# Kernel tuning notes

Measured on AMD Instinct MI355X. Metric: run time of the kernel, lower is better.

The kernel has to match this reference:

```python
import jax, jax.numpy as jnp
import numpy as np

N_NODES = 100000


def gcn_conv(x, edge_index, W, b, n):
    """PyG-style GCNConv: h = D^-1/2 (A + I) D^-1/2 (x W) + b."""
    h = x @ W  # [n, out]
    loops = jnp.arange(n, dtype=edge_index.dtype)
    src = jnp.concatenate([edge_index[0], loops])
    dst = jnp.concatenate([edge_index[1], loops])
    deg = jax.ops.segment_sum(jnp.ones_like(dst, dtype=h.dtype), dst, num_segments=n)
    dinv = jnp.where(deg > 0, jax.lax.rsqrt(deg), 0.0)
    norm = dinv[src] * dinv[dst]  # [E+n]
    msg = h[src] * norm[:, None]
    out = jax.ops.segment_sum(msg, dst, num_segments=n)
    return out + b


def setup_inputs() -> dict:
    key = jax.random.key(0)
    ks = jax.random.split(key, 12)
    n, f, hid, c, e = N_NODES, 128, 16, 32, 3200000
    x = jax.random.normal(ks[0], (n, f), dtype=jnp.float32)
    edge_index_pos = jax.random.randint(ks[1], (2, e), 0, n, dtype=jnp.int32)
    edge_index_neg = jax.random.randint(ks[2], (2, e), 0, n, dtype=jnp.int32)
    def glorot(k, fi, fo):
        lim = np.sqrt(6.0 / (fi + fo)).astype(np.float32)
        return jax.random.uniform(k, (fi, fo), minval=-lim, maxval=lim, dtype=jnp.float32)
    return {
        "x": x,
        "edge_index_pos": edge_index_pos,
        "edge_index_neg": edge_index_neg,
        "W1p": glorot(ks[3], f, hid), "b1p": jnp.zeros((hid,), jnp.float32),
        "W1n": glorot(ks[4], f, hid), "b1n": jnp.zeros((hid,), jnp.float32),
        "W2p": glorot(ks[5], hid, c), "b2p": jnp.zeros((c,), jnp.float32),
        "W2n": glorot(ks[6], hid, c), "b2n": jnp.zeros((c,), jnp.float32),
    }


def reference(x, edge_index_pos, edge_index_neg, W1p, b1p, W1n, b1n, W2p, b2p, W2n, b2n):
    n = x.shape[0]
    # layer 1: relu(pos) - relu(neg)
    h = (jax.nn.relu(gcn_conv(x, edge_index_pos, W1p, b1p, n))
         - jax.nn.relu(gcn_conv(x, edge_index_neg, W1n, b1n, n)))
    # dropout is identity in eval mode (training=False)
    h = (jax.nn.relu(gcn_conv(h, edge_index_pos, W2p, b2p, n))
         - jax.nn.relu(gcn_conv(h, edge_index_neg, W2n, b2n, n)))
    return jax.nn.log_softmax(h, axis=1)
```

## Files before the change

### kernel.cpp

```cpp
#include <hip/hip_runtime.h>
#include <hip/hip_fp16.h>


#define BSHIFT 8
#define BSZ 256
#define MAX_NBK 512
#define FILL_CAP 13056
#define SORT_CAP 12032

__device__ __forceinline__ int chunk_of_block(int bid, int NCH) {
  return (NCH % 8 == 0) ? (bid % 8) * (NCH / 8) + bid / 8 : bid;
}


__global__ __launch_bounds__(256) void bucket_count2(
    const int* __restrict__ eP, const int* __restrict__ eN,
    int E, int CH, int NCH, int NBK, int* __restrict__ ccP, int* __restrict__ ccN) {
  __shared__ int cnt[MAX_NBK];
  const int* dsts = (blockIdx.y ? eN : eP) + E;
  int* cc = blockIdx.y ? ccN : ccP;
  const int c = chunk_of_block(blockIdx.x, NCH);
  for (int i = threadIdx.x; i < NBK; i += 256) cnt[i] = 0;
  __syncthreads();
  int base = c * CH, end = min(E, base + CH);
  for (int idx = base + threadIdx.x; idx < end; idx += 256)
    atomicAdd(&cnt[dsts[idx] >> BSHIFT], 1);
  __syncthreads();
  for (int i = threadIdx.x; i < NBK; i += 256)
    cc[(size_t)c * NBK + i] = cnt[i];
}

__global__ __launch_bounds__(512) void col_scan2(
    int* __restrict__ ccP, int* __restrict__ ccN, int NCH, int NBK,
    int* __restrict__ totP, int* __restrict__ totN) {
  __shared__ int s[512];
  int* cc = blockIdx.y ? ccN : ccP;
  int* tot = blockIdx.y ? totN : totP;
  int b = blockIdx.x, t = threadIdx.x;
  int v = (t < NCH) ? cc[(size_t)t * NBK + b] : 0;
  s[t] = v;
  for (int off = 1; off < 512; off <<= 1) {
    __syncthreads();
    int a = (t >= off) ? s[t - off] : 0;
    __syncthreads();
    s[t] += a;
  }
  __syncthreads();
  if (t < NCH) cc[(size_t)t * NBK + b] = s[t] - v;
  if (t == 511) tot[b] = s[511];
}

__global__ __launch_bounds__(512) void base_scan(
    const int* __restrict__ totP, const int* __restrict__ totN, int NBK,
    int* __restrict__ baseP, int* __restrict__ baseN,
    int* __restrict__ rowP, int* __restrict__ rowN, int n, int E) {
  __shared__ int sp[512], sn[512];
  __shared__ int carryP, carryN;
  int t = threadIdx.x;
  if (t == 0) { carryP = 0; carryN = 0; }
  __syncthreads();
  for (int tile = 0; tile < NBK; tile += 512) {
    int idx = tile + t;
    int vp = (idx < NBK) ? totP[idx] : 0;
    int vn = (idx < NBK) ? totN[idx] : 0;
    sp[t] = vp; sn[t] = vn;
    for (int off = 1; off < 512; off <<= 1) {
      __syncthreads();
      int ap = (t >= off) ? sp[t - off] : 0;
      int an = (t >= off) ? sn[t - off] : 0;
      __syncthreads();
      sp[t] += ap; sn[t] += an;
    }
    __syncthreads();
    if (idx < NBK) {
      baseP[idx] = carryP + sp[t] - vp;
      baseN[idx] = carryN + sn[t] - vn;
    }
    __syncthreads();
    if (t == 0) { carryP += sp[511]; carryN += sn[511]; }
    __syncthreads();
  }
  if (t == 0) {
    baseP[NBK] = E; baseN[NBK] = E;
    rowP[n] = E; rowN[n] = E;
  }
}

__global__ __launch_bounds__(512) void bucket_fill3(
    const int* __restrict__ eP, const int* __restrict__ eN,
    int E, int CH, int NCH, int NBK,
    const int* __restrict__ ccP, const int* __restrict__ ccN,
    const int* __restrict__ totP, const int* __restrict__ totN,
    const int* __restrict__ basP, const int* __restrict__ basN,
    unsigned* __restrict__ prP, unsigned* __restrict__ prN) {
  __shared__ unsigned obuf[FILL_CAP];
  __shared__ int chofs[MAX_NBK], hist[MAX_NBK], lofs[MAX_NBK], cur[MAX_NBK];
  __shared__ int s[512];
  const int* edges = blockIdx.y ? eN : eP;
  const int* cc = blockIdx.y ? ccN : ccP;
  const int* tot = blockIdx.y ? totN : totP;
  const int* bas = blockIdx.y ? basN : basP;
  unsigned* pairs = blockIdx.y ? prN : prP;
  const int c = chunk_of_block(blockIdx.x, NCH);
  const int t = threadIdx.x;

  int h = 0;
  if (t < NBK) {
    int o0 = cc[(size_t)c * NBK + t];
    int o1 = (c + 1 < NCH) ? cc[(size_t)(c + 1) * NBK + t] : tot[t];
    chofs[t] = o0;
    h = o1 - o0;
    hist[t] = h;
  }
  s[t] = h;
  for (int off = 1; off < 512; off <<= 1) {
    __syncthreads();
    int a = (t >= off) ? s[t - off] : 0;
    __syncthreads();
    s[t] += a;
  }
  __syncthreads();
  if (t < NBK) { lofs[t] = s[t] - hist[t]; cur[t] = s[t] - hist[t]; }
  __syncthreads();

  int base = c * CH, end = min(E, base + CH);
  for (int idx = base + t; idx < end; idx += 512) {
    int sv = edges[idx], d = edges[E + idx];
    int b = d >> BSHIFT;
    int pos = atomicAdd(&cur[b], 1);
    obuf[pos] = (unsigned)sv | ((unsigned)(d & (BSZ - 1)) << 24);
  }
  __syncthreads();

  if (t < NBK) {
    int cnt = hist[t], lo = lofs[t];
    unsigned* dst = pairs + (size_t)bas[t] + chofs[t];
    for (int j = 0; j < cnt; ++j) dst[j] = obuf[lo + j];
  }
}

__global__ __launch_bounds__(256) void tile_sort3(
    const unsigned* __restrict__ prP, const unsigned* __restrict__ prN,
    const int* __restrict__ basP, const int* __restrict__ basN, int n,
    float* __restrict__ dinvP, float* __restrict__ dinvN,
    int* __restrict__ rowP, int* __restrict__ rowN,
    unsigned* __restrict__ srcsP, unsigned* __restrict__ srcsN) {
  __shared__ unsigned obuf[SORT_CAP];
  __shared__ int hist[BSZ];
  __shared__ int scn[BSZ];
  __shared__ int cur[BSZ];
  const unsigned* pairs = blockIdx.y ? prN : prP;
  const int* base = blockIdx.y ? basN : basP;
  float* dinv = blockIdx.y ? dinvN : dinvP;
  int* rowoff = blockIdx.y ? rowN : rowP;
  unsigned* srcs = blockIdx.y ? srcsN : srcsP;
  const int b = blockIdx.x, t = threadIdx.x;
  const int s0 = base[b], s1 = base[b + 1], cnt = s1 - s0;
  hist[t] = 0;
  __syncthreads();
  for (int i = s0 + t; i < s1; i += 256)
    atomicAdd(&hist[pairs[i] >> 24], 1);
  __syncthreads();
  scn[t] = hist[t];
  __syncthreads();
  for (int off = 1; off < BSZ; off <<= 1) {
    int v = (t >= off) ? scn[t - off] : 0;
    __syncthreads();
    scn[t] += v;
    __syncthreads();
  }
  {
    int excl = scn[t] - hist[t];
    cur[t] = excl;
    int node = b * BSZ + t;
    if (node < n) {
      rowoff[node] = s0 + excl;
      dinv[node] = rsqrtf(1.0f + (float)hist[t]);
    }
  }
  __syncthreads();
  if (cnt <= SORT_CAP) {
    for (int i = s0 + t; i < s1; i += 256) {
      unsigned p = pairs[i];
      int pos = atomicAdd(&cur[p >> 24], 1);
      obuf[pos] = p & 0xFFFFFFu;
    }
    __syncthreads();
    for (int i = t; i < cnt; i += 256) srcs[s0 + i] = obuf[i];
  } else {
    for (int i = s0 + t; i < s1; i += 256) {
      unsigned p = pairs[i];
      int pos = atomicAdd(&cur[p >> 24], 1);
      srcs[s0 + pos] = p & 0xFFFFFFu;
    }
  }
}

__global__ __launch_bounds__(256) void xw1_kernel(
    const float* __restrict__ x, const float* __restrict__ Wp, const float* __restrict__ Wn,
    const float* __restrict__ dinvP, const float* __restrict__ dinvN,
    __half* __restrict__ hp, __half* __restrict__ hn, int n)
{
  __shared__ float xs[16 * 132];
  __shared__ float wp[128 * 16], wn[128 * 16];
  const int tid = threadIdx.x;
  const int rowBase = blockIdx.x * 16;

  for (int idx = tid; idx < 512; idx += 256) {
    ((float4*)wp)[idx] = ((const float4*)Wp)[idx];
    ((float4*)wn)[idx] = ((const float4*)Wn)[idx];
  }
  const int nrows = min(16, n - rowBase);
  for (int idx = tid; idx < nrows * 32; idx += 256) {
    int r = idx >> 5, c4 = idx & 31;
    float4 v = ((const float4*)(x + (size_t)(rowBase + r) * 128))[c4];
    *(float4*)(xs + r * 132 + c4 * 4) = v;
  }
  __syncthreads();

  const int r = tid >> 4, c = tid & 15;
  const int i = rowBase + r;
  if (i < n) {
    float ap = 0.f, an = 0.f;
    #pragma unroll
    for (int k = 0; k < 128; ++k) {
      float xv = xs[r * 132 + k];
      ap += xv * wp[k * 16 + c];
      an += xv * wn[k * 16 + c];
    }
    hp[(size_t)i * 16 + c] = __float2half(ap * dinvP[i]);
    hn[(size_t)i * 16 + c] = __float2half(an * dinvN[i]);
  }
}

__device__ __forceinline__ void fma_mix2(float& aLo, float& aHi, unsigned h2, float one) {
  asm("v_fma_mix_f32 %0, %2, %3, %0 op_sel:[0,0,0] op_sel_hi:[1,0,0]\n\t"
      "v_fma_mix_f32 %1, %2, %3, %1 op_sel:[1,0,0] op_sel_hi:[1,0,0]"
      : "+v"(aLo), "+v"(aHi)
      : "v"(h2), "v"(one));
}

__device__ __forceinline__ void seg_sum4(
    const unsigned* __restrict__ srcs, int e, int e1,
    const __half* __restrict__ tab, int lane4, float one,
    float& f0, float& f1, float& f2, float& f3)
{
  float g0 = 0.f, g1 = 0.f, g2 = 0.f, g3 = 0.f;
  for (; e + 8 <= e1; e += 8) {
    unsigned a[8];
    #pragma unroll
    for (int j = 0; j < 8; ++j) a[j] = srcs[e + j];
    uint2 v[8];
    #pragma unroll
    for (int j = 0; j < 8; ++j)
      v[j] = *(const uint2*)(tab + (size_t)a[j] * 16 + lane4 * 4);
    #pragma unroll
    for (int j = 0; j < 8; j += 2) {
      fma_mix2(f0, f1, v[j].x, one);
      fma_mix2(f2, f3, v[j].y, one);
      fma_mix2(g0, g1, v[j + 1].x, one);
      fma_mix2(g2, g3, v[j + 1].y, one);
    }
  }
  for (; e + 2 <= e1; e += 2) {
    unsigned a0 = srcs[e], a1 = srcs[e + 1];
    uint2 v0 = *(const uint2*)(tab + (size_t)a0 * 16 + lane4 * 4);
    uint2 v1 = *(const uint2*)(tab + (size_t)a1 * 16 + lane4 * 4);
    fma_mix2(f0, f1, v0.x, one);
    fma_mix2(f2, f3, v0.y, one);
    fma_mix2(g0, g1, v1.x, one);
    fma_mix2(g2, g3, v1.y, one);
  }
  if (e < e1) {
    uint2 v = *(const uint2*)(tab + (size_t)srcs[e] * 16 + lane4 * 4);
    fma_mix2(f0, f1, v.x, one);
    fma_mix2(f2, f3, v.y, one);
  }
  f0 += g0; f1 += g1; f2 += g2; f3 += g3;
}

__global__ __launch_bounds__(256) void agg_split(
    const unsigned* __restrict__ srcP, const int* __restrict__ rowP,
    const unsigned* __restrict__ srcN, const int* __restrict__ rowN,
    const __half* __restrict__ inP, const __half* __restrict__ inN,
    const float* __restrict__ dinvP, const float* __restrict__ dinvN,
    float* __restrict__ tmpP, float* __restrict__ tmpN, int n)
{
  const int gb = blockIdx.x;
  const int xcd = gb & 7;
  const int sign = xcd >> 2;
  const int nblk = (gb >> 3) * 4 + (xcd & 3);
  const int lane4 = threadIdx.x & 3, grp = threadIdx.x >> 2;
  const int i = nblk * 64 + grp;
  if (i >= n) return;

  const unsigned* srcs = sign ? srcN : srcP;
  const int* row = sign ? rowN : rowP;
  const __half* tab = sign ? inN : inP;
  const float* dinv = sign ? dinvN : dinvP;
  float* tmp = sign ? tmpN : tmpP;

  const float one = 1.0f;
  float f0 = 0.f, f1 = 0.f, f2 = 0.f, f3 = 0.f;
  uint2 self = *(const uint2*)(tab + (size_t)i * 16 + lane4 * 4);
  fma_mix2(f0, f1, self.x, one);
  fma_mix2(f2, f3, self.y, one);
  seg_sum4(srcs, row[i], row[i + 1], tab, lane4, one, f0, f1, f2, f3);
  const float d = dinv[i];
  float4 o;
  o.x = f0 * d; o.y = f1 * d; o.z = f2 * d; o.w = f3 * d;
  *(float4*)(tmp + (size_t)i * 16 + lane4 * 4) = o;
}

__global__ __launch_bounds__(256) void combine1(
    const float* __restrict__ tmpP, const float* __restrict__ tmpN,
    const float* __restrict__ bp, const float* __restrict__ bn,
    const float* __restrict__ dinvP, const float* __restrict__ dinvN,
    __half* __restrict__ Gp, __half* __restrict__ Gn, long long total)
{
  long long j = (long long)blockIdx.x * 256 + threadIdx.x;
  if (j >= total) return;
  int i = (int)(j >> 4), lane = (int)(j & 15);
  float ap = bp[lane] + tmpP[j];
  float an = bn[lane] + tmpN[j];
  float h = fmaxf(ap, 0.f) - fmaxf(an, 0.f);
  Gp[j] = __float2half(h * dinvP[i]);
  Gn[j] = __float2half(h * dinvN[i]);
}

__global__ __launch_bounds__(256) void final2(
    const float* __restrict__ Up, const float* __restrict__ Un,
    const float* __restrict__ W2p, const float* __restrict__ W2n,
    const float* __restrict__ b2p, const float* __restrict__ b2n,
    float* __restrict__ out, int n)
{
  __shared__ float wp[16 * 32], wn[16 * 32];
  for (int i = threadIdx.x; i < 512; i += 256) { wp[i] = W2p[i]; wn[i] = W2n[i]; }
  __syncthreads();

  const int tid = threadIdx.x;
  const int lane = tid & 15, grp = tid >> 4;
  const int i = blockIdx.x * 16 + grp;
  if (i >= n) return;

  float tp = Up[(size_t)i * 16 + lane];
  float tn = Un[(size_t)i * 16 + lane];

  float ap0 = b2p[lane], ap1 = b2p[lane + 16];
  float an0 = b2n[lane], an1 = b2n[lane + 16];
  #pragma unroll
  for (int k = 0; k < 16; ++k) {
    float tpk = __shfl(tp, k, 16);
    float tnk = __shfl(tn, k, 16);
    ap0 += tpk * wp[k * 32 + lane];
    ap1 += tpk * wp[k * 32 + lane + 16];
    an0 += tnk * wn[k * 32 + lane];
    an1 += tnk * wn[k * 32 + lane + 16];
  }
  float v0 = fmaxf(ap0, 0.f) - fmaxf(an0, 0.f);
  float v1 = fmaxf(ap1, 0.f) - fmaxf(an1, 0.f);
  float m = fmaxf(v0, v1);
  #pragma unroll
  for (int off = 8; off > 0; off >>= 1) m = fmaxf(m, __shfl_xor(m, off, 16));
  float s = __expf(v0 - m) + __expf(v1 - m);
  #pragma unroll
  for (int off = 8; off > 0; off >>= 1) s += __shfl_xor(s, off, 16);
  float ls = __logf(s);
  out[(size_t)i * 32 + lane] = v0 - m - ls;
  out[(size_t)i * 32 + lane + 16] = v1 - m - ls;
}

extern "C" void kernel_launch(void* const* d_in, const int* in_sizes, int n_in,
                              void* d_out, int out_size, void* d_ws, size_t ws_size,
                              hipStream_t stream) {
  const float* x   = (const float*)d_in[0];
  const int*   eP  = (const int*)d_in[1];
  const int*   eN  = (const int*)d_in[2];
  const float* W1p = (const float*)d_in[3];
  const float* b1p = (const float*)d_in[4];
  const float* W1n = (const float*)d_in[5];
  const float* b1n = (const float*)d_in[6];
  const float* W2p = (const float*)d_in[7];
  const float* b2p = (const float*)d_in[8];
  const float* W2n = (const float*)d_in[9];
  const float* b2n = (const float*)d_in[10];
  float* out = (float*)d_out;

  const int HID = in_sizes[4];
  const int F   = in_sizes[3] / HID;
  const int n   = in_sizes[0] / F;
  const int E   = in_sizes[1] / 2;
  (void)out_size; (void)n_in; (void)ws_size;

  const int NBK = (n + BSZ - 1) >> BSHIFT;
  const int CH  = (((E + 255) / 256) + 255) & ~255;
  const int NCH = (E + CH - 1) / CH;

  char* p = (char*)d_ws;
  auto alloc = [&](size_t bytes) { char* r = p; p += (bytes + 255) & ~(size_t)255; return r; };

  int*      ccP   = (int*)alloc((size_t)NCH * NBK * 4);
  int*      ccN   = (int*)alloc((size_t)NCH * NBK * 4);
  int*      totP  = (int*)alloc((size_t)NBK * 4);
  int*      totN  = (int*)alloc((size_t)NBK * 4);
  int*      basP  = (int*)alloc((size_t)(NBK + 1) * 4);
  int*      basN  = (int*)alloc((size_t)(NBK + 1) * 4);
  unsigned* prP   = (unsigned*)alloc((size_t)E * 4);
  unsigned* prN   = (unsigned*)alloc((size_t)E * 4);
  unsigned* srcP  = (unsigned*)alloc((size_t)E * 4);
  unsigned* srcN  = (unsigned*)alloc((size_t)E * 4);
  int*      rowP  = (int*)alloc((size_t)(n + 1) * 4);
  int*      rowN  = (int*)alloc((size_t)(n + 1) * 4);
  float*    dinvP = (float*)alloc((size_t)n * 4);
  float*    dinvN = (float*)alloc((size_t)n * 4);
  __half*   hsP   = (__half*)alloc((size_t)n * 16 * 2);
  __half*   hsN   = (__half*)alloc((size_t)n * 16 * 2);
  __half*   Gp    = (__half*)alloc((size_t)n * 16 * 2);
  __half*   Gn    = (__half*)alloc((size_t)n * 16 * 2);
  float*    tmpP  = (float*)alloc((size_t)n * 16 * 4);
  float*    tmpN  = (float*)alloc((size_t)n * 16 * 4);

  hipLaunchKernelGGL(bucket_count2, dim3(NCH, 2), dim3(256), 0, stream,
                     eP, eN, E, CH, NCH, NBK, ccP, ccN);
  hipLaunchKernelGGL(col_scan2, dim3(NBK, 2), dim3(512), 0, stream,
                     ccP, ccN, NCH, NBK, totP, totN);
  hipLaunchKernelGGL(base_scan, dim3(1), dim3(512), 0, stream,
                     totP, totN, NBK, basP, basN, rowP, rowN, n, E);
  hipLaunchKernelGGL(bucket_fill3, dim3(NCH, 2), dim3(512), 0, stream,
                     eP, eN, E, CH, NCH, NBK, ccP, ccN, totP, totN,
                     basP, basN, prP, prN);
  hipLaunchKernelGGL(tile_sort3, dim3(NBK, 2), dim3(256), 0, stream,
                     prP, prN, basP, basN, n, dinvP, dinvN, rowP, rowN, srcP, srcN);

  const int NB16 = (n + 15) / 16;
  const int NB64 = (n + 63) / 64;
  const int NBS  = ((NB64 + 3) / 4) * 4;
  const int GRID = NBS * 2;

  hipLaunchKernelGGL(xw1_kernel, dim3(NB16), dim3(256), 0, stream,
                     x, W1p, W1n, dinvP, dinvN, hsP, hsN, n);
  hipLaunchKernelGGL(agg_split, dim3(GRID), dim3(256), 0, stream,
                     srcP, rowP, srcN, rowN, hsP, hsN, dinvP, dinvN, tmpP, tmpN, n);
  hipLaunchKernelGGL(combine1, dim3((int)(((long long)n * 16 + 255) / 256)), dim3(256), 0, stream,
                     tmpP, tmpN, b1p, b1n, dinvP, dinvN, Gp, Gn, (long long)n * 16);

  hipLaunchKernelGGL(agg_split, dim3(GRID), dim3(256), 0, stream,
                     srcP, rowP, srcN, rowN, Gp, Gn, dinvP, dinvN, tmpP, tmpN, n);
  hipLaunchKernelGGL(final2, dim3(NB16), dim3(256), 0, stream,
                     tmpP, tmpN, W2p, W2n, b2p, b2n, out, n);
}
```

Measured before the change: 241.1 us.

## Fold base scan into fill/sort kernels, vectorize edge loads, coalesce bucket writeback

Removes the single-block base_scan launch. bucket_fill3 now recomputes the bucket prefix locally, and tile_sort3 derives its start offset by reducing the preceding bucket totals. Edge loads in count and fill use nontemporal 4-wide loads. The per-bucket writeback in fill is spread across a wavefront instead of one thread per bucket, giving coalesced stores. combine1 is vectorized to float4 with packed half2 stores, and nontemporal hints are added to the aggregation loads and stores. The trade-off is redundant prefix work in every block; the tile_sort reduction grows with the bucket index, up to about 391 buckets.

```diff
diff --git a/kernel.cpp b/kernel.cpp
--- a/kernel.cpp
+++ b/kernel.cpp
@@ -7,6 +7,9 @@
 #define MAX_NBK 512
 #define FILL_CAP 13056
 #define SORT_CAP 12032
+
+typedef int   i32x4 __attribute__((ext_vector_type(4)));
+typedef float f32x4 __attribute__((ext_vector_type(4)));
 
 __device__ __forceinline__ int chunk_of_block(int bid, int NCH) {
   return (NCH % 8 == 0) ? (bid % 8) * (NCH / 8) + bid / 8 : bid;
@@ -23,8 +26,17 @@
   for (int i = threadIdx.x; i < NBK; i += 256) cnt[i] = 0;
   __syncthreads();
   int base = c * CH, end = min(E, base + CH);
-  for (int idx = base + threadIdx.x; idx < end; idx += 256)
-    atomicAdd(&cnt[dsts[idx] >> BSHIFT], 1);
+  for (int idx = base + threadIdx.x * 4; idx < end; idx += 1024) {
+    if (idx + 4 <= end) {
+      i32x4 d = __builtin_nontemporal_load((const i32x4*)(dsts + idx));
+      atomicAdd(&cnt[d.x >> BSHIFT], 1);
+      atomicAdd(&cnt[d.y >> BSHIFT], 1);
+      atomicAdd(&cnt[d.z >> BSHIFT], 1);
+      atomicAdd(&cnt[d.w >> BSHIFT], 1);
+    } else {
+      for (int k = idx; k < end; ++k) atomicAdd(&cnt[dsts[k] >> BSHIFT], 1);
+    }
+  }
   __syncthreads();
   for (int i = threadIdx.x; i < NBK; i += 256)
     cc[(size_t)c * NBK + i] = cnt[i];
@@ -50,56 +62,19 @@
   if (t == 511) tot[b] = s[511];
 }
 
-__global__ __launch_bounds__(512) void base_scan(
-    const int* __restrict__ totP, const int* __restrict__ totN, int NBK,
-    int* __restrict__ baseP, int* __restrict__ baseN,
-    int* __restrict__ rowP, int* __restrict__ rowN, int n, int E) {
-  __shared__ int sp[512], sn[512];
-  __shared__ int carryP, carryN;
-  int t = threadIdx.x;
-  if (t == 0) { carryP = 0; carryN = 0; }
-  __syncthreads();
-  for (int tile = 0; tile < NBK; tile += 512) {
-    int idx = tile + t;
-    int vp = (idx < NBK) ? totP[idx] : 0;
-    int vn = (idx < NBK) ? totN[idx] : 0;
-    sp[t] = vp; sn[t] = vn;
-    for (int off = 1; off < 512; off <<= 1) {
-      __syncthreads();
-      int ap = (t >= off) ? sp[t - off] : 0;
-      int an = (t >= off) ? sn[t - off] : 0;
-      __syncthreads();
-      sp[t] += ap; sn[t] += an;
-    }
-    __syncthreads();
-    if (idx < NBK) {
-      baseP[idx] = carryP + sp[t] - vp;
-      baseN[idx] = carryN + sn[t] - vn;
-    }
-    __syncthreads();
-    if (t == 0) { carryP += sp[511]; carryN += sn[511]; }
-    __syncthreads();
-  }
-  if (t == 0) {
-    baseP[NBK] = E; baseN[NBK] = E;
-    rowP[n] = E; rowN[n] = E;
-  }
-}
-
 __global__ __launch_bounds__(512) void bucket_fill3(
     const int* __restrict__ eP, const int* __restrict__ eN,
     int E, int CH, int NCH, int NBK,
     const int* __restrict__ ccP, const int* __restrict__ ccN,
     const int* __restrict__ totP, const int* __restrict__ totN,
-    const int* __restrict__ basP, const int* __restrict__ basN,
     unsigned* __restrict__ prP, unsigned* __restrict__ prN) {
   __shared__ unsigned obuf[FILL_CAP];
   __shared__ int chofs[MAX_NBK], hist[MAX_NBK], lofs[MAX_NBK], cur[MAX_NBK];
+  __shared__ int bas_l[MAX_NBK];
   __shared__ int s[512];
   const int* edges = blockIdx.y ? eN : eP;
   const int* cc = blockIdx.y ? ccN : ccP;
   const int* tot = blockIdx.y ? totN : totP;
-  const int* bas = blockIdx.y ? basN : basP;
   unsigned* pairs = blockIdx.y ? prN : prP;
   const int c = chunk_of_block(blockIdx.x, NCH);
   const int t = threadIdx.x;
@@ -123,25 +98,52 @@
   if (t < NBK) { lofs[t] = s[t] - hist[t]; cur[t] = s[t] - hist[t]; }
   __syncthreads();
 
+  int tv = (t < NBK) ? tot[t] : 0;
+  s[t] = tv;
+  for (int off = 1; off < 512; off <<= 1) {
+    __syncthreads();
+    int a = (t >= off) ? s[t - off] : 0;
+    __syncthreads();
+    s[t] += a;
+  }
+  __syncthreads();
+  if (t < NBK) bas_l[t] = s[t] - tv;
+  __syncthreads();
+
   int base = c * CH, end = min(E, base + CH);
-  for (int idx = base + t; idx < end; idx += 512) {
-    int sv = edges[idx], d = edges[E + idx];
-    int b = d >> BSHIFT;
-    int pos = atomicAdd(&cur[b], 1);
-    obuf[pos] = (unsigned)sv | ((unsigned)(d & (BSZ - 1)) << 24);
-  }
-  __syncthreads();
-
-  if (t < NBK) {
-    int cnt = hist[t], lo = lofs[t];
-    unsigned* dst = pairs + (size_t)bas[t] + chofs[t];
-    for (int j = 0; j < cnt; ++j) dst[j] = obuf[lo + j];
+  for (int idx = base + t * 4; idx < end; idx += 2048) {
+    if (idx + 4 <= end) {
+      i32x4 sv = __builtin_nontemporal_load((const i32x4*)(edges + idx));
+      i32x4 dv = __builtin_nontemporal_load((const i32x4*)(edges + E + idx));
+      int p0 = atomicAdd(&cur[dv.x >> BSHIFT], 1);
+      obuf[p0] = (unsigned)sv.x | ((unsigned)(dv.x & (BSZ - 1)) << 24);
+      int p1 = atomicAdd(&cur[dv.y >> BSHIFT], 1);
+      obuf[p1] = (unsigned)sv.y | ((unsigned)(dv.y & (BSZ - 1)) << 24);
+      int p2 = atomicAdd(&cur[dv.z >> BSHIFT], 1);
+      obuf[p2] = (unsigned)sv.z | ((unsigned)(dv.z & (BSZ - 1)) << 24);
+      int p3 = atomicAdd(&cur[dv.w >> BSHIFT], 1);
+      obuf[p3] = (unsigned)sv.w | ((unsigned)(dv.w & (BSZ - 1)) << 24);
+    } else {
+      for (int k = idx; k < end; ++k) {
+        int sv = edges[k], d = edges[E + k];
+        int pos = atomicAdd(&cur[d >> BSHIFT], 1);
+        obuf[pos] = (unsigned)sv | ((unsigned)(d & (BSZ - 1)) << 24);
+      }
+    }
+  }
+  __syncthreads();
+
+  const int wv = t >> 6, ln = t & 63;
+  for (int b = wv; b < NBK; b += 8) {
+    int cnt2 = hist[b], lo = lofs[b];
+    unsigned* dst = pairs + (size_t)bas_l[b] + chofs[b];
+    for (int j = ln; j < cnt2; j += 64) dst[j] = obuf[lo + j];
   }
 }
 
 __global__ __launch_bounds__(256) void tile_sort3(
     const unsigned* __restrict__ prP, const unsigned* __restrict__ prN,
-    const int* __restrict__ basP, const int* __restrict__ basN, int n,
+    const int* __restrict__ totP, const int* __restrict__ totN, int n, int E,
     float* __restrict__ dinvP, float* __restrict__ dinvN,
     int* __restrict__ rowP, int* __restrict__ rowN,
     unsigned* __restrict__ srcsP, unsigned* __restrict__ srcsN) {
@@ -149,17 +151,31 @@
   __shared__ int hist[BSZ];
   __shared__ int scn[BSZ];
   __shared__ int cur[BSZ];
+  __shared__ int red[256];
   const unsigned* pairs = blockIdx.y ? prN : prP;
-  const int* base = blockIdx.y ? basN : basP;
+  const int* tot = blockIdx.y ? totN : totP;
   float* dinv = blockIdx.y ? dinvN : dinvP;
   int* rowoff = blockIdx.y ? rowN : rowP;
   unsigned* srcs = blockIdx.y ? srcsN : srcsP;
   const int b = blockIdx.x, t = threadIdx.x;
-  const int s0 = base[b], s1 = base[b + 1], cnt = s1 - s0;
+
+  int part = 0;
+  for (int j = t; j < b; j += 256) part += tot[j];
+  red[t] = part;
+  __syncthreads();
+  for (int off = 128; off > 0; off >>= 1) {
+    if (t < off) red[t] += red[t + off];
+    __syncthreads();
+  }
+  const int s0 = red[0];
+  const int cnt = tot[b];
+  const int s1 = s0 + cnt;
+  if (b == (int)gridDim.x - 1 && t == 0) rowoff[n] = E;
+
   hist[t] = 0;
   __syncthreads();
   for (int i = s0 + t; i < s1; i += 256)
-    atomicAdd(&hist[pairs[i] >> 24], 1);
+    atomicAdd(&hist[__builtin_nontemporal_load(pairs + i) >> 24], 1);
   __syncthreads();
   scn[t] = hist[t];
   __syncthreads();
@@ -181,7 +197,7 @@
   __syncthreads();
   if (cnt <= SORT_CAP) {
     for (int i = s0 + t; i < s1; i += 256) {
-      unsigned p = pairs[i];
+      unsigned p = __builtin_nontemporal_load(pairs + i);
       int pos = atomicAdd(&cur[p >> 24], 1);
       obuf[pos] = p & 0xFFFFFFu;
     }
@@ -189,7 +205,7 @@
     for (int i = t; i < cnt; i += 256) srcs[s0 + i] = obuf[i];
   } else {
     for (int i = s0 + t; i < s1; i += 256) {
-      unsigned p = pairs[i];
+      unsigned p = __builtin_nontemporal_load(pairs + i);
       int pos = atomicAdd(&cur[p >> 24], 1);
       srcs[s0 + pos] = p & 0xFFFFFFu;
     }
@@ -249,7 +265,7 @@
   for (; e + 8 <= e1; e += 8) {
     unsigned a[8];
     #pragma unroll
-    for (int j = 0; j < 8; ++j) a[j] = srcs[e + j];
+    for (int j = 0; j < 8; ++j) a[j] = __builtin_nontemporal_load(srcs + e + j);
     uint2 v[8];
     #pragma unroll
     for (int j = 0; j < 8; ++j)
@@ -263,7 +279,8 @@
     }
   }
   for (; e + 2 <= e1; e += 2) {
-    unsigned a0 = srcs[e], a1 = srcs[e + 1];
+    unsigned a0 = __builtin_nontemporal_load(srcs + e);
+    unsigned a1 = __builtin_nontemporal_load(srcs + e + 1);
     uint2 v0 = *(const uint2*)(tab + (size_t)a0 * 16 + lane4 * 4);
     uint2 v1 = *(const uint2*)(tab + (size_t)a1 * 16 + lane4 * 4);
     fma_mix2(f0, f1, v0.x, one);
@@ -272,7 +289,8 @@
     fma_mix2(g2, g3, v1.y, one);
   }
   if (e < e1) {
-    uint2 v = *(const uint2*)(tab + (size_t)srcs[e] * 16 + lane4 * 4);
+    unsigned a0 = __builtin_nontemporal_load(srcs + e);
+    uint2 v = *(const uint2*)(tab + (size_t)a0 * 16 + lane4 * 4);
     fma_mix2(f0, f1, v.x, one);
     fma_mix2(f2, f3, v.y, one);
   }
@@ -294,11 +312,11 @@
   const int i = nblk * 64 + grp;
   if (i >= n) return;
 
-  const unsigned* srcs = sign ? srcN : srcP;
-  const int* row = sign ? rowN : rowP;
-  const __half* tab = sign ? inN : inP;
-  const float* dinv = sign ? dinvN : dinvP;
-  float* tmp = sign ? tmpN : tmpP;
+  const unsigned* __restrict__ srcs = sign ? srcN : srcP;
+  const int* __restrict__ row = sign ? rowN : rowP;
+  const __half* __restrict__ tab = sign ? inN : inP;
+  const float* __restrict__ dinv = sign ? dinvN : dinvP;
+  float* __restrict__ tmp = sign ? tmpN : tmpP;
 
   const float one = 1.0f;
   float f0 = 0.f, f1 = 0.f, f2 = 0.f, f3 = 0.f;
@@ -307,25 +325,35 @@
   fma_mix2(f2, f3, self.y, one);
   seg_sum4(srcs, row[i], row[i + 1], tab, lane4, one, f0, f1, f2, f3);
   const float d = dinv[i];
-  float4 o;
-  o.x = f0 * d; o.y = f1 * d; o.z = f2 * d; o.w = f3 * d;
-  *(float4*)(tmp + (size_t)i * 16 + lane4 * 4) = o;
+  f32x4 o = {f0 * d, f1 * d, f2 * d, f3 * d};
+  __builtin_nontemporal_store(o, (f32x4*)(tmp + (size_t)i * 16 + lane4 * 4));
 }
 
 __global__ __launch_bounds__(256) void combine1(
     const float* __restrict__ tmpP, const float* __restrict__ tmpN,
     const float* __restrict__ bp, const float* __restrict__ bn,
     const float* __restrict__ dinvP, const float* __restrict__ dinvN,
-    __half* __restrict__ Gp, __half* __restrict__ Gn, long long total)
+    __half* __restrict__ Gp, __half* __restrict__ Gn, int nq)
 {
-  long long j = (long long)blockIdx.x * 256 + threadIdx.x;
-  if (j >= total) return;
-  int i = (int)(j >> 4), lane = (int)(j & 15);
-  float ap = bp[lane] + tmpP[j];
-  float an = bn[lane] + tmpN[j];
-  float h = fmaxf(ap, 0.f) - fmaxf(an, 0.f);
-  Gp[j] = __float2half(h * dinvP[i]);
-  Gn[j] = __float2half(h * dinvN[i]);
+  int q = blockIdx.x * 256 + threadIdx.x;
+  if (q >= nq) return;
+  int i = q >> 2;
+  float4 tp = ((const float4*)tmpP)[q];
+  float4 tn = ((const float4*)tmpN)[q];
+  float4 bpv = ((const float4*)bp)[q & 3];
+  float4 bnv = ((const float4*)bn)[q & 3];
+  float dp = dinvP[i], dn = dinvN[i];
+  float h0 = fmaxf(bpv.x + tp.x, 0.f) - fmaxf(bnv.x + tn.x, 0.f);
+  float h1 = fmaxf(bpv.y + tp.y, 0.f) - fmaxf(bnv.y + tn.y, 0.f);
+  float h2 = fmaxf(bpv.z + tp.z, 0.f) - fmaxf(bnv.z + tn.z, 0.f);
+  float h3 = fmaxf(bpv.w + tp.w, 0.f) - fmaxf(bnv.w + tn.w, 0.f);
+  union { uint2 u; __half2 h[2]; } a, b;
+  a.h[0] = __floats2half2_rn(h0 * dp, h1 * dp);
+  a.h[1] = __floats2half2_rn(h2 * dp, h3 * dp);
+  b.h[0] = __floats2half2_rn(h0 * dn, h1 * dn);
+  b.h[1] = __floats2half2_rn(h2 * dn, h3 * dn);
+  ((uint2*)Gp)[q] = a.u;
+  ((uint2*)Gn)[q] = b.u;
 }
 
 __global__ __launch_bounds__(256) void final2(
@@ -403,8 +431,6 @@
   int*      ccN   = (int*)alloc((size_t)NCH * NBK * 4);
   int*      totP  = (int*)alloc((size_t)NBK * 4);
   int*      totN  = (int*)alloc((size_t)NBK * 4);
-  int*      basP  = (int*)alloc((size_t)(NBK + 1) * 4);
-  int*      basN  = (int*)alloc((size_t)(NBK + 1) * 4);
   unsigned* prP   = (unsigned*)alloc((size_t)E * 4);
   unsigned* prN   = (unsigned*)alloc((size_t)E * 4);
   unsigned* srcP  = (unsigned*)alloc((size_t)E * 4);
@@ -424,13 +450,10 @@
                      eP, eN, E, CH, NCH, NBK, ccP, ccN);
   hipLaunchKernelGGL(col_scan2, dim3(NBK, 2), dim3(512), 0, stream,
                      ccP, ccN, NCH, NBK, totP, totN);
-  hipLaunchKernelGGL(base_scan, dim3(1), dim3(512), 0, stream,
-                     totP, totN, NBK, basP, basN, rowP, rowN, n, E);
   hipLaunchKernelGGL(bucket_fill3, dim3(NCH, 2), dim3(512), 0, stream,
-                     eP, eN, E, CH, NCH, NBK, ccP, ccN, totP, totN,
-                     basP, basN, prP, prN);
+                     eP, eN, E, CH, NCH, NBK, ccP, ccN, totP, totN, prP, prN);
   hipLaunchKernelGGL(tile_sort3, dim3(NBK, 2), dim3(256), 0, stream,
-                     prP, prN, basP, basN, n, dinvP, dinvN, rowP, rowN, srcP, srcN);
+                     prP, prN, totP, totN, n, E, dinvP, dinvN, rowP, rowN, srcP, srcN);
 
   const int NB16 = (n + 15) / 16;
   const int NB64 = (n + 63) / 64;
@@ -441,8 +464,8 @@
                      x, W1p, W1n, dinvP, dinvN, hsP, hsN, n);
   hipLaunchKernelGGL(agg_split, dim3(GRID), dim3(256), 0, stream,
                      srcP, rowP, srcN, rowN, hsP, hsN, dinvP, dinvN, tmpP, tmpN, n);
-  hipLaunchKernelGGL(combine1, dim3((int)(((long long)n * 16 + 255) / 256)), dim3(256), 0, stream,
-                     tmpP, tmpN, b1p, b1n, dinvP, dinvN, Gp, Gn, (long long)n * 16);
+  hipLaunchKernelGGL(combine1, dim3((n * 4 + 255) / 256), dim3(256), 0, stream,
+                     tmpP, tmpN, b1p, b1n, dinvP, dinvN, Gp, Gn, n * 4);
 
   hipLaunchKernelGGL(agg_split, dim3(GRID), dim3(256), 0, stream,
                      srcP, rowP, srcN, rowN, Gp, Gn, dinvP, dinvN, tmpP, tmpN, n);
```

Measured after the change: 275.1 us. +14.1%, slower.
